# Performance work log

Hardware: AMD Instinct MI355X
Metric: run time of the kernel (lower is better)

The kernel has to match this reference:

```python
import jax, jax.numpy as jnp
import numpy as np

HEADS = 4
DIM_HEAD = 32
SCALE = 10.0
EPS = 1e-12


def setup_inputs() -> dict:
    key = jax.random.key(0)
    k1, k2, k3 = jax.random.split(key, 3)
    B, D, H, W, C = 2, 8, 16, 32, 128
    dim = HEADS * DIM_HEAD  # 128
    x = jax.random.normal(k1, (B, D, H, W, C), dtype=jnp.float32)
    # 1x1x1 convs are matmuls over the channel dim
    w_qkv = jax.random.normal(k2, (C, 3 * dim), dtype=jnp.float32) * (1.0 / np.sqrt(C))
    w_out = jax.random.normal(k3, (dim, C), dtype=jnp.float32) * (1.0 / np.sqrt(dim))
    b_out = jnp.zeros((C,), dtype=jnp.float32)
    return {"x": x, "w_qkv": w_qkv, "w_out": w_out, "b_out": b_out}


def reference(x, w_qkv, w_out, b_out):
    B, D, H, W, C = x.shape
    N = D * H * W
    dim = HEADS * DIM_HEAD
    xf = x.reshape(B, N, C)
    qkv = xf @ w_qkv                                   # [B, N, 3*dim]
    q, k, v = jnp.split(qkv, 3, axis=-1)
    def to_heads(t):
        return t.reshape(B, N, HEADS, DIM_HEAD)        # [B, N, h, d]
    q, k, v = to_heads(q), to_heads(k), to_heads(v)
    # L2-normalize q and k along head dim (cosine attention)
    q = q / jnp.clip(jnp.linalg.norm(q, axis=-1, keepdims=True), EPS)
    k = k / jnp.clip(jnp.linalg.norm(k, axis=-1, keepdims=True), EPS)
    sim = jnp.einsum('bihd,bjhd->bhij', q, k) * SCALE  # [B, h, N, N]
    attn = jax.nn.softmax(sim, axis=-1)
    out = jnp.einsum('bhij,bjhd->bihd', attn, v)       # [B, N, h, d]
    out = out.reshape(B, N, dim)
    out = out @ w_out + b_out                          # [B, N, C]
    return out.reshape(B, D, H, W, C)
```

## Files before the change

### kernel.cpp

```cpp
#include <hip/hip_runtime.h>
#include <math.h>

#define HEADS   4
#define DH      32
#define NB      4096
#define BATCH   2
#define C_IN    128
#define QKV_COLS 384
#define TOTROWS 8192
#define ATT_EPS 1e-12f
#define C1      14.42695040888963f
#define QROWS   8
#define OROWS   8

typedef __attribute__((ext_vector_type(16))) float f32x16;
typedef _Float16 f16x8 __attribute__((ext_vector_type(8)));
typedef __fp16 fp16x2 __attribute__((ext_vector_type(2)));
typedef unsigned short u16;

__device__ __forceinline__ u16 f16b(float a) {
  union { _Float16 h; u16 u; } t; t.h = (_Float16)a; return t.u;
}
__device__ __forceinline__ unsigned pkf16rtn(float a, float b) {
  return (unsigned)f16b(a) | ((unsigned)f16b(b) << 16);
}
union Uh2 { fp16x2 h; unsigned u; };
__device__ __forceinline__ unsigned pkf16(float a, float b) {
  Uh2 t; t.h = __builtin_amdgcn_cvt_pkrtz(a, b); return t.u;
}
union U8h { unsigned u[4]; f16x8 h8; };
__device__ __forceinline__ f16x8 mk8h(unsigned a, unsigned b, unsigned c, unsigned d) {
  U8h t; t.u[0] = a; t.u[1] = b; t.u[2] = c; t.u[3] = d; return t.h8;
}
__device__ __forceinline__ void pl32swap(unsigned& a, unsigned& b) {
  asm("v_permlane32_swap_b32 %0, %1" : "+v"(a), "+v"(b));
}
#define GL16(gp, lp)                                                        \
  __builtin_amdgcn_global_load_lds(                                         \
      (const __attribute__((address_space(1))) void*)(gp),                  \
      (__attribute__((address_space(3))) void*)(lp), 16, 0, 0)

__global__ __launch_bounds__(384) void qkv_kernel(
    const float* __restrict__ x, const float* __restrict__ w,
    float* __restrict__ Qs, u16* __restrict__ K16, u16* __restrict__ VT16) {
  const int tid = threadIdx.x;
  const int r0  = blockIdx.x * QROWS;

  float4 a4[QROWS];
#pragma unroll
  for (int r = 0; r < QROWS; ++r) a4[r] = make_float4(0.f, 0.f, 0.f, 0.f);

  for (int c4 = 0; c4 < 32; ++c4) {
    const float wv0 = w[(c4 * 4 + 0) * QKV_COLS + tid];
    const float wv1 = w[(c4 * 4 + 1) * QKV_COLS + tid];
    const float wv2 = w[(c4 * 4 + 2) * QKV_COLS + tid];
    const float wv3 = w[(c4 * 4 + 3) * QKV_COLS + tid];
#pragma unroll
    for (int r = 0; r < QROWS; ++r) {
      const float* xr = x + (size_t)(r0 + r) * C_IN + c4 * 4;
      a4[r].x = fmaf(xr[0], wv0, a4[r].x);
      a4[r].y = fmaf(xr[1], wv1, a4[r].y);
      a4[r].z = fmaf(xr[2], wv2, a4[r].z);
      a4[r].w = fmaf(xr[3], wv3, a4[r].w);
    }
  }

  float acc[QROWS];
#pragma unroll
  for (int r = 0; r < QROWS; ++r)
    acc[r] = (a4[r].x + a4[r].y) + (a4[r].z + a4[r].w);

  const int part = tid >> 7;
  if (part < 2) {
#pragma unroll
    for (int r = 0; r < QROWS; ++r) {
      float s = acc[r] * acc[r];
      s += __shfl_xor(s, 1, 32);
      s += __shfl_xor(s, 2, 32);
      s += __shfl_xor(s, 4, 32);
      s += __shfl_xor(s, 8, 32);
      s += __shfl_xor(s, 16, 32);
      acc[r] *= 1.0f / fmaxf(sqrtf(s), ATT_EPS);
    }
  }

  const int h = (tid >> 5) & 3, d = tid & 31;
  const int b = r0 >> 12, n0 = r0 & (NB - 1);
  const int bh = b * HEADS + h;
  if (part == 0) {
    float* dst = Qs + ((size_t)bh * NB + n0) * DH + d;
#pragma unroll
    for (int r = 0; r < QROWS; ++r) dst[(size_t)r * DH] = acc[r] * C1;
  } else if (part == 1) {
    const size_t kb = ((size_t)bh * NB + n0) * DH + d;
#pragma unroll
    for (int r = 0; r < QROWS; ++r) K16[kb + (size_t)r * DH] = f16b(acc[r]);
  } else {
    const size_t vb = ((size_t)bh * DH + d) * NB + n0;
#pragma unroll
    for (int r = 0; r < QROWS; r += 4) {
      uint2 hv;
      hv.x = pkf16rtn(acc[r + 0], acc[r + 1]);
      hv.y = pkf16rtn(acc[r + 2], acc[r + 3]);
      *(uint2*)(VT16 + vb + r) = hv;
    }
  }
}

__global__ __launch_bounds__(512, 4) void attn_kernel(
    const float* __restrict__ Qs, const u16* __restrict__ K16,
    const u16* __restrict__ VT16, float* __restrict__ AO) {
  __shared__ __align__(16) char sbuf[2][4][4][2048];

  const int tid  = threadIdx.x;
  const int lane = tid & 63;
  const int w    = tid >> 6;
  const int su   = w & 3;
  const int u    = w >> 2;
  const int q    = lane & 31;
  const int hi   = lane >> 5;
  const int bh   = blockIdx.x & 7;
  const int qp   = blockIdx.x >> 3;

  const int nrow = qp * 64 + u * 32 + q;
  const float* qrow = Qs + ((size_t)bh * NB + nrow) * DH;
  f16x8 fq16[2];
#pragma unroll
  for (int sl = 0; sl < 2; ++sl) {
    const int d0 = sl * 16 + hi * 8;
    const float4 a = *(const float4*)(qrow + d0);
    const float4 b = *(const float4*)(qrow + d0 + 4);
    fq16[sl] = mk8h(pkf16rtn(a.x, a.y), pkf16rtn(a.z, a.w),
                    pkf16rtn(b.x, b.y), pkf16rtn(b.z, b.w));
  }

  const u16* gp[4]; int gst[4], ldso[4];
#pragma unroll
  for (int it = 0; it < 4; ++it) {
    const int i    = tid + it * 512;
    const int pidx = i >> 7;
    const int sp   = pidx >> 2;
    const int code = pidx & 3;
    const int pl   = code >> 1;
    const int sub  = code & 1;
    const int s    = i & 127;
    const int rtt  = s >> 2;
    const int ps   = s & 3;
    const int slot = ((ps ^ ((rtt >> 1) & 3)) << 3);
    if (pl == 0) {
      gp[it]  = K16 + (size_t)bh * NB * DH
                    + (size_t)(sp * 1024 + sub * 32 + rtt) * DH + slot;
      gst[it] = 64 * DH;
    } else {
      gp[it]  = VT16 + (size_t)bh * DH * NB + (size_t)rtt * NB
                     + sp * 1024 + sub * 32 + slot;
      gst[it] = 64;
    }
    ldso[it] = i * 16;
  }
  char* const sb = (char*)sbuf;
  auto stage = [&](int buf) {
#pragma unroll
    for (int it = 0; it < 4; ++it) {
      GL16(gp[it], sb + buf * 32768 + ldso[it]);
      gp[it] += gst[it];
    }
  };

  const int swq = (q >> 1) & 3;
  int koff[2];
#pragma unroll
  for (int i = 0; i < 2; ++i) koff[i] = q * 64 + (((i * 2 + hi) ^ swq) << 4);

  f32x16 oa, zz;
#pragma unroll
  for (int r = 0; r < 16; ++r) { oa[r] = 0.f; zz[r] = 0.f; }
  float lrun = 0.f;

  stage(0);
  __syncthreads();

  for (int t = 0; t < 16; ++t) {
    const int cur = t & 1;
    if (t < 15) stage(cur ^ 1);

    const char* cb = sb + cur * 32768 + su * 8192;

#pragma unroll
    for (int sub = 0; sub < 2; ++sub) {
      const char* ck = cb + sub * 2048;
      const char* cv = cb + 4096 + sub * 2048;

      f32x16 sa;
      __builtin_amdgcn_s_setprio(1);
      {
        const f16x8 fk0 = *(const f16x8*)(ck + koff[0]);
        const f16x8 fk1 = *(const f16x8*)(ck + koff[1]);
        sa = __builtin_amdgcn_mfma_f32_32x32x16_f16(fk0, fq16[0], zz, 0, 0, 0);
        sa = __builtin_amdgcn_mfma_f32_32x32x16_f16(fk1, fq16[1], sa, 0, 0, 0);
      }
      __builtin_amdgcn_s_setprio(0);

      float e[16], lsum = 0.f;
#pragma unroll
      for (int r = 0; r < 16; ++r) {
        e[r] = __builtin_amdgcn_exp2f(sa[r]);
        lsum += e[r];
      }
      lrun += lsum;

      __builtin_amdgcn_s_setprio(1);
#pragma unroll
      for (int m = 0; m < 2; ++m) {
        const float* eb = e + 8 * m;
        unsigned x0 = pkf16(eb[0], eb[1]), x1 = pkf16(eb[2], eb[3]);
        unsigned y0 = pkf16(eb[4], eb[5]), y1 = pkf16(eb[6], eb[7]);
        pl32swap(x0, y0);
        pl32swap(x1, y1);
        const f16x8 fP = mk8h(x0, x1, y0, y1);
        const f16x8 fv = *(const f16x8*)(cv + koff[m]);
        oa = __builtin_amdgcn_mfma_f32_32x32x16_f16(fv, fP, oa, 0, 0, 0);
      }
      __builtin_amdgcn_s_setprio(0);
    }
    __syncthreads();
  }

  float* const mO = (float*)sbuf;
  float* const mL = mO + 2 * 3 * 32 * 33;
  const float Lfull = lrun + __shfl_xor(lrun, 32);
  if (su != 0) {
    const int sidx = (u * 3 + (su - 1)) * 32 + q;
    if (hi == 0) mL[sidx] = Lfull;
#pragma unroll
    for (int r = 0; r < 16; ++r) {
      const int d = (r & 3) + 8 * (r >> 2) + 4 * hi;
      mO[sidx * 33 + d] = oa[r];
    }
  }
  __syncthreads();
  if (su == 0) {
    float Lt = Lfull;
#pragma unroll
    for (int s = 0; s < 3; ++s) Lt += mL[(u * 3 + s) * 32 + q];
    const float inv = 1.0f / Lt;
    const int b = bh >> 2, h = bh & 3;
    float* dst = AO + ((size_t)(b * NB + nrow)) * 128 + h * DH;
#pragma unroll
    for (int r = 0; r < 16; ++r) {
      const int d = (r & 3) + 8 * (r >> 2) + 4 * hi;
      float v = oa[r];
#pragma unroll
      for (int s = 0; s < 3; ++s) v += mO[((u * 3 + s) * 32 + q) * 33 + d];
      dst[d] = v * inv;
    }
  }
}

__global__ __launch_bounds__(128) void outproj_kernel(
    const float* __restrict__ AO, const float* __restrict__ w,
    const float* __restrict__ bias, float* __restrict__ out) {
  const int tid = threadIdx.x;
  const int r0  = blockIdx.x * OROWS;

  float4 a4[OROWS];
#pragma unroll
  for (int r = 0; r < OROWS; ++r) a4[r] = make_float4(0.f, 0.f, 0.f, 0.f);

  for (int c4 = 0; c4 < 32; ++c4) {
    const float wv0 = w[(c4 * 4 + 0) * 128 + tid];
    const float wv1 = w[(c4 * 4 + 1) * 128 + tid];
    const float wv2 = w[(c4 * 4 + 2) * 128 + tid];
    const float wv3 = w[(c4 * 4 + 3) * 128 + tid];
#pragma unroll
    for (int r = 0; r < OROWS; ++r) {
      const float* xr = AO + (size_t)(r0 + r) * 128 + c4 * 4;
      a4[r].x = fmaf(xr[0], wv0, a4[r].x);
      a4[r].y = fmaf(xr[1], wv1, a4[r].y);
      a4[r].z = fmaf(xr[2], wv2, a4[r].z);
      a4[r].w = fmaf(xr[3], wv3, a4[r].w);
    }
  }

  __syncthreads();

  const float bv = bias[tid];
#pragma unroll
  for (int r = 0; r < OROWS; ++r) {
    const float acc = (a4[r].x + a4[r].y) + (a4[r].z + a4[r].w);
    out[(size_t)(r0 + r) * 128 + tid] = acc + bv;
  }
}

extern "C" void kernel_launch(void* const* d_in, const int* in_sizes, int n_in,
                              void* d_out, int out_size, void* d_ws, size_t ws_size,
                              hipStream_t stream) {
  (void)in_sizes; (void)n_in; (void)out_size; (void)ws_size;
  const float* x     = (const float*)d_in[0];
  const float* w_qkv = (const float*)d_in[1];
  const float* w_out = (const float*)d_in[2];
  const float* b_out = (const float*)d_in[3];
  float* out = (float*)d_out;

  float* ws = (float*)d_ws;
  float* Qs = ws;
  u16* K16  = (u16*)(ws + 1048576);
  u16* VT16 = K16 + 1048576;
  float* AO = out;

  qkv_kernel<<<TOTROWS / QROWS, 384, 0, stream>>>(x, w_qkv, Qs, K16, VT16);
  attn_kernel<<<512, 512, 0, stream>>>(Qs, K16, VT16, AO);
  outproj_kernel<<<TOTROWS / OROWS, 128, 0, stream>>>(AO, w_out, b_out, out);
}
```

Baseline: 66.74 us.

## Load K and V fragments directly from global memory instead of LDS staging

Removes the double-buffered LDS staging of K/V tiles (global_load_lds plus __syncthreads per tile). Each wave now reads its K and V^T MFMA fragments straight from global memory into registers, stepping 32 keys per iteration over its 1024-key slice. This drops the block-wide barriers and shrinks LDS use to the merge buffers. In exchange, the loads are exposed in every iteration with only unroll-2 to hide latency, and the V^T reads become strided 16-byte accesses per lane.

Result: slower. 81.87 us (+22.7%).

```diff
diff --git a/kernel.cpp b/kernel.cpp
--- a/kernel.cpp
+++ b/kernel.cpp
@@ -35,10 +35,6 @@
 __device__ __forceinline__ void pl32swap(unsigned& a, unsigned& b) {
   asm("v_permlane32_swap_b32 %0, %1" : "+v"(a), "+v"(b));
 }
-#define GL16(gp, lp)                                                        \
-  __builtin_amdgcn_global_load_lds(                                         \
-      (const __attribute__((address_space(1))) void*)(gp),                  \
-      (__attribute__((address_space(3))) void*)(lp), 16, 0, 0)
 
 __global__ __launch_bounds__(384) void qkv_kernel(
     const float* __restrict__ x, const float* __restrict__ w,
@@ -110,7 +106,9 @@
 __global__ __launch_bounds__(512, 4) void attn_kernel(
     const float* __restrict__ Qs, const u16* __restrict__ K16,
     const u16* __restrict__ VT16, float* __restrict__ AO) {
-  __shared__ __align__(16) char sbuf[2][4][4][2048];
+  __shared__ float mrg[2 * 3 * 32 * 33 + 2 * 3 * 32];
+  float* const mO = mrg;
+  float* const mL = mrg + 2 * 3 * 32 * 33;
 
   const int tid  = threadIdx.x;
   const int lane = tid & 63;
@@ -134,100 +132,55 @@
                     pkf16rtn(b.x, b.y), pkf16rtn(b.z, b.w));
   }
 
-  const u16* gp[4]; int gst[4], ldso[4];
-#pragma unroll
-  for (int it = 0; it < 4; ++it) {
-    const int i    = tid + it * 512;
-    const int pidx = i >> 7;
-    const int sp   = pidx >> 2;
-    const int code = pidx & 3;
-    const int pl   = code >> 1;
-    const int sub  = code & 1;
-    const int s    = i & 127;
-    const int rtt  = s >> 2;
-    const int ps   = s & 3;
-    const int slot = ((ps ^ ((rtt >> 1) & 3)) << 3);
-    if (pl == 0) {
-      gp[it]  = K16 + (size_t)bh * NB * DH
-                    + (size_t)(sp * 1024 + sub * 32 + rtt) * DH + slot;
-      gst[it] = 64 * DH;
-    } else {
-      gp[it]  = VT16 + (size_t)bh * DH * NB + (size_t)rtt * NB
-                     + sp * 1024 + sub * 32 + slot;
-      gst[it] = 64;
-    }
-    ldso[it] = i * 16;
-  }
-  char* const sb = (char*)sbuf;
-  auto stage = [&](int buf) {
-#pragma unroll
-    for (int it = 0; it < 4; ++it) {
-      GL16(gp[it], sb + buf * 32768 + ldso[it]);
-      gp[it] += gst[it];
-    }
-  };
-
-  const int swq = (q >> 1) & 3;
-  int koff[2];
-#pragma unroll
-  for (int i = 0; i < 2; ++i) koff[i] = q * 64 + (((i * 2 + hi) ^ swq) << 4);
+  const u16* kp = K16 + (size_t)bh * NB * DH + (size_t)(su * 1024 + q) * DH + hi * 8;
+  const u16* vp = VT16 + (size_t)bh * DH * NB + (size_t)q * NB + su * 1024 + hi * 8;
 
   f32x16 oa, zz;
 #pragma unroll
   for (int r = 0; r < 16; ++r) { oa[r] = 0.f; zz[r] = 0.f; }
   float lrun = 0.f;
 
-  stage(0);
-  __syncthreads();
-
-  for (int t = 0; t < 16; ++t) {
-    const int cur = t & 1;
-    if (t < 15) stage(cur ^ 1);
-
-    const char* cb = sb + cur * 32768 + su * 8192;
-
-#pragma unroll
-    for (int sub = 0; sub < 2; ++sub) {
-      const char* ck = cb + sub * 2048;
-      const char* cv = cb + 4096 + sub * 2048;
-
-      f32x16 sa;
-      __builtin_amdgcn_s_setprio(1);
-      {
-        const f16x8 fk0 = *(const f16x8*)(ck + koff[0]);
-        const f16x8 fk1 = *(const f16x8*)(ck + koff[1]);
-        sa = __builtin_amdgcn_mfma_f32_32x32x16_f16(fk0, fq16[0], zz, 0, 0, 0);
-        sa = __builtin_amdgcn_mfma_f32_32x32x16_f16(fk1, fq16[1], sa, 0, 0, 0);
-      }
-      __builtin_amdgcn_s_setprio(0);
-
-      float e[16], lsum = 0.f;
-#pragma unroll
-      for (int r = 0; r < 16; ++r) {
-        e[r] = __builtin_amdgcn_exp2f(sa[r]);
-        lsum += e[r];
-      }
-      lrun += lsum;
-
-      __builtin_amdgcn_s_setprio(1);
-#pragma unroll
-      for (int m = 0; m < 2; ++m) {
-        const float* eb = e + 8 * m;
-        unsigned x0 = pkf16(eb[0], eb[1]), x1 = pkf16(eb[2], eb[3]);
-        unsigned y0 = pkf16(eb[4], eb[5]), y1 = pkf16(eb[6], eb[7]);
-        pl32swap(x0, y0);
-        pl32swap(x1, y1);
-        const f16x8 fP = mk8h(x0, x1, y0, y1);
-        const f16x8 fv = *(const f16x8*)(cv + koff[m]);
-        oa = __builtin_amdgcn_mfma_f32_32x32x16_f16(fv, fP, oa, 0, 0, 0);
-      }
-      __builtin_amdgcn_s_setprio(0);
-    }
-    __syncthreads();
-  }
-
-  float* const mO = (float*)sbuf;
-  float* const mL = mO + 2 * 3 * 32 * 33;
+#pragma unroll 2
+  for (int t = 0; t < 32; ++t) {
+    const f16x8 fk0 = *(const f16x8*)(kp);
+    const f16x8 fk1 = *(const f16x8*)(kp + 16);
+    const f16x8 fv0 = *(const f16x8*)(vp);
+    const f16x8 fv1 = *(const f16x8*)(vp + 16);
+    kp += 32 * DH;
+    vp += 32;
+
+    f32x16 sa;
+    __builtin_amdgcn_s_setprio(1);
+    sa = __builtin_amdgcn_mfma_f32_32x32x16_f16(fk0, fq16[0], zz, 0, 0, 0);
+    sa = __builtin_amdgcn_mfma_f32_32x32x16_f16(fk1, fq16[1], sa, 0, 0, 0);
+    __builtin_amdgcn_s_setprio(0);
+
+    float e[16], lsum = 0.f;
+#pragma unroll
+    for (int r = 0; r < 16; ++r) {
+      e[r] = __builtin_amdgcn_exp2f(sa[r]);
+      lsum += e[r];
+    }
+    lrun += lsum;
+
+    __builtin_amdgcn_s_setprio(1);
+    {
+      unsigned x0 = pkf16(e[0], e[1]), x1 = pkf16(e[2], e[3]);
+      unsigned y0 = pkf16(e[4], e[5]), y1 = pkf16(e[6], e[7]);
+      pl32swap(x0, y0);
+      pl32swap(x1, y1);
+      oa = __builtin_amdgcn_mfma_f32_32x32x16_f16(fv0, mk8h(x0, x1, y0, y1),
+                                                  oa, 0, 0, 0);
+      unsigned z0 = pkf16(e[8], e[9]),  z1 = pkf16(e[10], e[11]);
+      unsigned t0 = pkf16(e[12], e[13]), t1 = pkf16(e[14], e[15]);
+      pl32swap(z0, t0);
+      pl32swap(z1, t1);
+      oa = __builtin_amdgcn_mfma_f32_32x32x16_f16(fv1, mk8h(z0, z1, t0, t1),
+                                                  oa, 0, 0, 0);
+    }
+    __builtin_amdgcn_s_setprio(0);
+  }
+
   const float Lfull = lrun + __shfl_xor(lrun, 32);
   if (su != 0) {
     const int sidx = (u * 3 + (su - 1)) * 32 + q;
```
